# Performance work log

Measured on AMD Instinct MI355X. Metric: run time of the kernel, lower is better.

Reference implementation:

```python
import jax, jax.numpy as jnp
import numpy as np

N_GRAPH_NODES = 100000  # size of g.ndata['centrality']
N_GRAPH_EDGES = 3200000


def setup_inputs() -> dict:
    key = jax.random.key(0)
    k1, k2, k3, k4 = jax.random.split(key, 4)
    n_node, n_path, l_path = 100000, 32, 8
    paths = jax.random.randint(k1, (n_node, n_path, l_path), 0, N_GRAPH_NODES, dtype=jnp.int32)
    edge_ids = jax.random.randint(k2, (n_node, n_path, l_path - 1), 0, N_GRAPH_EDGES, dtype=jnp.int32)
    rand_lens = jax.random.randint(k3, (n_node, n_path), 0, l_path, dtype=jnp.int32)
    centrality = jax.random.uniform(k4, (N_GRAPH_NODES,), dtype=jnp.float32)
    return {"paths": paths, "edge_ids": edge_ids, "rand_lens": rand_lens,
            "centrality": centrality, "k_path": 8}


def reference(paths, edge_ids, rand_lens, centrality, k_path):
    # paths: [n_node, n_path, l_path] node ids; edge_ids: [n_node, n_path, l_path-1]
    n_node, n_path, l_path = paths.shape
    n_graph = centrality.shape[0]

    # meta_mask[r, j] = (j > r)  (strict upper triangle); paths[mask] = -1
    pos = jnp.arange(l_path, dtype=rand_lens.dtype)  # [l_path]
    masked_paths = jnp.where(pos > rand_lens[..., None], jnp.int32(-1), paths)

    # centrality padded with a trailing zero so id -1 (-> index n_graph) scores 0
    cent_pad = jnp.concatenate([centrality, jnp.zeros((1,), centrality.dtype)])
    gather_idx = jnp.where(masked_paths < 0, n_graph, masked_paths)
    scores = jnp.sum(cent_pad[gather_idx], axis=-1)  # [n_node, n_path]

    # top-k paths per start node by summed centrality
    _, topk_idx = jax.lax.top_k(scores, k_path)  # [n_node, k_path]
    paths_sel = jnp.take_along_axis(masked_paths, topk_idx[:, :, None], axis=1)   # [n_node, k_path, l_path]
    edge_ids_sel = jnp.take_along_axis(edge_ids, topk_idx[:, :, None], axis=1)    # [n_node, k_path, l_path-1]
    return paths_sel, edge_ids_sel
```

## Files before the change

### kernel.cpp

```cpp
#include <hip/hip_runtime.h>


#define N_NODE   100000
#define N_PATH   32
#define L_PATH   8
#define K_PATH   8

__global__ __launch_bounds__(256) void path_sampling_kernel(
    const int*   __restrict__ paths,
    const int*   __restrict__ edge_ids,
    const int*   __restrict__ rand_lens,
    const float* __restrict__ centrality,
    int*         __restrict__ out_paths,
    int*         __restrict__ out_edges)
{
    const int t    = threadIdx.x;
    const int path = t & 31;
    const int node = blockIdx.x * 8 + (t >> 5);
    if (node >= N_NODE) return;

    const size_t row = (size_t)node * N_PATH + path;

    const int4* p4 = (const int4*)(paths + row * L_PATH);
    int4 pa = p4[0];
    int4 pb = p4[1];
    int  len = rand_lens[row];

    int mp[8] = {pa.x, pa.y, pa.z, pa.w, pb.x, pb.y, pb.z, pb.w};

    float c[8];
    #pragma unroll
    for (int j = 0; j < 8; ++j) {
        if (j > len) mp[j] = -1;
        c[j] = (mp[j] < 0) ? 0.0f : centrality[mp[j]];
    }

    const float score = ((c[0] + c[1]) + (c[2] + c[3]))
                      + ((c[4] + c[5]) + (c[6] + c[7]));

    int rank = 0;
    #pragma unroll
    for (int j = 0; j < 32; ++j) {
        float sj = __shfl(score, j, 32);
        rank += (sj > score) || (sj == score && j < path);
    }

    if (rank < K_PATH) {
        const size_t obase = (size_t)node * K_PATH + rank;

        int4* op = (int4*)(out_paths + obase * L_PATH);
        op[0] = make_int4(mp[0], mp[1], mp[2], mp[3]);
        op[1] = make_int4(mp[4], mp[5], mp[6], mp[7]);

        const int* esrc = edge_ids + row * (L_PATH - 1);
        int*       edst = out_edges + obase * (L_PATH - 1);
        #pragma unroll
        for (int j = 0; j < L_PATH - 1; ++j) edst[j] = esrc[j];
    }
}

extern "C" void kernel_launch(void* const* d_in, const int* in_sizes, int n_in,
                              void* d_out, int out_size, void* d_ws, size_t ws_size,
                              hipStream_t stream) {
    const int*   paths      = (const int*)  d_in[0];
    const int*   edge_ids   = (const int*)  d_in[1];
    const int*   rand_lens  = (const int*)  d_in[2];
    const float* centrality = (const float*)d_in[3];

    int* out_paths = (int*)d_out;
    int* out_edges = out_paths + (size_t)N_NODE * K_PATH * L_PATH;

    const int nodes_per_block = 8;
    const int grid = (N_NODE + nodes_per_block - 1) / nodes_per_block;

    path_sampling_kernel<<<grid, 256, 0, stream>>>(
        paths, edge_ids, rand_lens, centrality, out_paths, out_edges);
}
```

Baseline: 75.28 us.

## Coalesce edge-id copy via shared-memory rank map and use nontemporal loads/stores

Each winning path now records its lane in shared memory by rank, and after a barrier all 32 lanes of a node cooperatively copy the 56 selected edge ids with contiguous, coalesced stores instead of 8 lanes each writing 7 strided ints. Path loads and output stores use nontemporal builtins to avoid polluting cache with streaming data. The bounds check is removed and the grid uses exact division, which relies on N_NODE being a multiple of 8, and a block-wide barrier is added.

```diff
diff --git a/kernel.cpp b/kernel.cpp
--- a/kernel.cpp
+++ b/kernel.cpp
@@ -5,6 +5,8 @@
 #define N_PATH   32
 #define L_PATH   8
 #define K_PATH   8
+
+typedef int v4i __attribute__((ext_vector_type(4)));
 
 __global__ __launch_bounds__(256) void path_sampling_kernel(
     const int*   __restrict__ paths,
@@ -14,17 +16,19 @@
     int*         __restrict__ out_paths,
     int*         __restrict__ out_edges)
 {
+    __shared__ int wsrc[8][8];
+
     const int t    = threadIdx.x;
-    const int path = t & 31;
-    const int node = blockIdx.x * 8 + (t >> 5);
-    if (node >= N_NODE) return;
+    const int lane = t & 31;
+    const int n8   = t >> 5;
+    const int node = blockIdx.x * 8 + n8;
 
-    const size_t row = (size_t)node * N_PATH + path;
+    const size_t row = (size_t)node * N_PATH + lane;
 
-    const int4* p4 = (const int4*)(paths + row * L_PATH);
-    int4 pa = p4[0];
-    int4 pb = p4[1];
-    int  len = rand_lens[row];
+    const v4i* p4 = (const v4i*)(paths + row * L_PATH);
+    v4i pa = __builtin_nontemporal_load(p4);
+    v4i pb = __builtin_nontemporal_load(p4 + 1);
+    int len = rand_lens[row];
 
     int mp[8] = {pa.x, pa.y, pa.z, pa.w, pb.x, pb.y, pb.z, pb.w};
 
@@ -42,20 +46,40 @@
     #pragma unroll
     for (int j = 0; j < 32; ++j) {
         float sj = __shfl(score, j, 32);
-        rank += (sj > score) || (sj == score && j < path);
+        rank += (sj > score) || (sj == score && j < lane);
     }
 
     if (rank < K_PATH) {
+        wsrc[n8][rank] = lane;
+
         const size_t obase = (size_t)node * K_PATH + rank;
+        v4i* op = (v4i*)(out_paths + obase * L_PATH);
+        v4i lo = {mp[0], mp[1], mp[2], mp[3]};
+        v4i hi = {mp[4], mp[5], mp[6], mp[7]};
+        __builtin_nontemporal_store(lo, op);
+        __builtin_nontemporal_store(hi, op + 1);
+    }
 
-        int4* op = (int4*)(out_paths + obase * L_PATH);
-        op[0] = make_int4(mp[0], mp[1], mp[2], mp[3]);
-        op[1] = make_int4(mp[4], mp[5], mp[6], mp[7]);
+    __syncthreads();
 
-        const int* esrc = edge_ids + row * (L_PATH - 1);
-        int*       edst = out_edges + obase * (L_PATH - 1);
-        #pragma unroll
-        for (int j = 0; j < L_PATH - 1; ++j) edst[j] = esrc[j];
+    const int* ebase = edge_ids + (size_t)node * (N_PATH * (L_PATH - 1));
+    int*       edst  = out_edges + (size_t)node * (K_PATH * (L_PATH - 1));
+
+    {
+        const int f   = lane;
+        const int r   = f / 7;
+        const int col = f - r * 7;
+        const int srow = wsrc[n8][r];
+        int v = __builtin_nontemporal_load(ebase + srow * 7 + col);
+        __builtin_nontemporal_store(v, edst + f);
+    }
+    if (lane < 24) {
+        const int f   = lane + 32;
+        const int r   = f / 7;
+        const int col = f - r * 7;
+        const int srow = wsrc[n8][r];
+        int v = __builtin_nontemporal_load(ebase + srow * 7 + col);
+        __builtin_nontemporal_store(v, edst + f);
     }
 }
 
@@ -71,7 +95,7 @@
     int* out_edges = out_paths + (size_t)N_NODE * K_PATH * L_PATH;
 
     const int nodes_per_block = 8;
-    const int grid = (N_NODE + nodes_per_block - 1) / nodes_per_block;
+    const int grid = N_NODE / nodes_per_block;
 
     path_sampling_kernel<<<grid, 256, 0, stream>>>(
         paths, edge_ids, rand_lens, centrality, out_paths, out_edges);
```

Measured after the change: 110.7 us. 1.47x slower.

## Map one node per wavefront, split paths across half-waves, coalesce edge copy

Applied to the files above, without the earlier changes.

Each 64-lane wavefront now handles one node, with two lanes per path that each load and score half of the path. Partial scores are combined with a cross-half shuffle, and the ranking reads all 32 scores from shared memory as vectors instead of doing 32 shuffles. Winning path indices are stored in shared memory so 56 lanes can copy the selected edge rows with contiguous stores, replacing the old per-thread copy of 7 scattered words. There is no barrier between the shared-memory writes and reads; it relies on the wavefront running in lockstep, and the grid assumes N_NODE is divisible by 4.

```diff
diff --git a/kernel.cpp b/kernel.cpp
--- a/kernel.cpp
+++ b/kernel.cpp
@@ -5,6 +5,9 @@
 #define N_PATH   32
 #define L_PATH   8
 #define K_PATH   8
+
+typedef int   v4i __attribute__((ext_vector_type(4)));
+typedef float v4f __attribute__((ext_vector_type(4)));
 
 __global__ __launch_bounds__(256) void path_sampling_kernel(
     const int*   __restrict__ paths,
@@ -14,48 +17,62 @@
     int*         __restrict__ out_paths,
     int*         __restrict__ out_edges)
 {
+    __shared__ float ssc[4][32];
+    __shared__ int   wsrc[4][8];
+
     const int t    = threadIdx.x;
-    const int path = t & 31;
-    const int node = blockIdx.x * 8 + (t >> 5);
-    if (node >= N_NODE) return;
+    const int wv   = t >> 6;
+    const int lane = t & 63;
+    const int half = lane >> 5;
+    const int p    = lane & 31;
+    const int node = blockIdx.x * 4 + wv;
 
-    const size_t row = (size_t)node * N_PATH + path;
+    const size_t row = (size_t)node * N_PATH + p;
 
-    const int4* p4 = (const int4*)(paths + row * L_PATH);
-    int4 pa = p4[0];
-    int4 pb = p4[1];
-    int  len = rand_lens[row];
+    v4i mp4 = ((const v4i*)paths)[row * 2 + half];
+    int len = rand_lens[row];
 
-    int mp[8] = {pa.x, pa.y, pa.z, pa.w, pb.x, pb.y, pb.z, pb.w};
+    int mp[4] = {mp4.x, mp4.y, mp4.z, mp4.w};
 
-    float c[8];
+    const int jb = half * 4;
+    float c[4];
     #pragma unroll
-    for (int j = 0; j < 8; ++j) {
-        if (j > len) mp[j] = -1;
-        c[j] = (mp[j] < 0) ? 0.0f : centrality[mp[j]];
+    for (int k = 0; k < 4; ++k) {
+        if (jb + k > len) mp[k] = -1;
+        c[k] = (mp[k] < 0) ? 0.0f : centrality[mp[k]];
     }
 
-    const float score = ((c[0] + c[1]) + (c[2] + c[3]))
-                      + ((c[4] + c[5]) + (c[6] + c[7]));
+    const float ps    = (c[0] + c[1]) + (c[2] + c[3]);
+    const float other = __shfl_xor(ps, 32);
+    const float s     = ps + other;
 
+    if (!half) ssc[wv][p] = s;
+    v4f sc[8];
+    #pragma unroll
+    for (int i = 0; i < 8; ++i) sc[i] = ((const v4f*)ssc[wv])[i];
+
+    const unsigned ltm = (1u << p) - 1u;
     int rank = 0;
     #pragma unroll
     for (int j = 0; j < 32; ++j) {
-        float sj = __shfl(score, j, 32);
-        rank += (sj > score) || (sj == score && j < path);
+        const float sj = sc[j >> 2][j & 3];
+        rank += (sj > s) || ((sj == s) && ((ltm >> j) & 1u));
     }
 
     if (rank < K_PATH) {
         const size_t obase = (size_t)node * K_PATH + rank;
+        v4i m = {mp[0], mp[1], mp[2], mp[3]};
+        ((v4i*)out_paths)[obase * 2 + half] = m;
+        if (!half) wsrc[wv][rank] = p;
+    }
 
-        int4* op = (int4*)(out_paths + obase * L_PATH);
-        op[0] = make_int4(mp[0], mp[1], mp[2], mp[3]);
-        op[1] = make_int4(mp[4], mp[5], mp[6], mp[7]);
-
-        const int* esrc = edge_ids + row * (L_PATH - 1);
-        int*       edst = out_edges + obase * (L_PATH - 1);
-        #pragma unroll
-        for (int j = 0; j < L_PATH - 1; ++j) edst[j] = esrc[j];
+    const int* ebase = edge_ids + (size_t)node * (N_PATH * (L_PATH - 1));
+    int*       edst  = out_edges + (size_t)node * (K_PATH * (L_PATH - 1));
+    if (lane < 56) {
+        const int r    = lane / 7;
+        const int col  = lane - r * 7;
+        const int srow = wsrc[wv][r];
+        edst[lane] = ebase[srow * 7 + col];
     }
 }
 
@@ -70,8 +87,8 @@
     int* out_paths = (int*)d_out;
     int* out_edges = out_paths + (size_t)N_NODE * K_PATH * L_PATH;
 
-    const int nodes_per_block = 8;
-    const int grid = (N_NODE + nodes_per_block - 1) / nodes_per_block;
+    const int nodes_per_block = 4;
+    const int grid = N_NODE / nodes_per_block;
 
     path_sampling_kernel<<<grid, 256, 0, stream>>>(
         paths, edge_ids, rand_lens, centrality, out_paths, out_edges);
```

Result: slower. 78.29 us, median of 3 (+4.0%).
